# Optimization experiments

Hardware: AMD Instinct MI355X
Metric: run time of the kernel (lower is better)

## Reference

```python
import math
import jax, jax.numpy as jnp
import numpy as np

N_HEAD = 16
N_EMBD = 2048
HEAD_DIM = N_EMBD // N_HEAD  # 128
ROPE_BASE = 10000.0
EPS = 1e-12  # F.normalize eps


def setup_inputs() -> dict:
    key = jax.random.key(0)
    ks = jax.random.split(key, 5)
    B, T, C = 2, 2048, N_EMBD
    s = 0.02
    return {
        "x": jax.random.normal(ks[0], (B, T, C), jnp.float32),
        "Wq": jax.random.normal(ks[1], (C, C), jnp.float32) * s,
        "Wk": jax.random.normal(ks[2], (C, C), jnp.float32) * s,
        "Wv": jax.random.normal(ks[3], (C, C), jnp.float32) * s,
        "Wo": jax.random.normal(ks[4], (C, C), jnp.float32) * s,
        "qk_scale": jnp.ones((HEAD_DIM,), jnp.float32) / math.sqrt(N_EMBD),
    }


def _rope(x, cos, sin):
    # x: [B,T,H,D], cos/sin: [T, D/2] broadcast as [1,T,1,D/2]
    d = x.shape[-1] // 2
    x1, x2 = x[..., :d], x[..., d:]
    c = cos[None, :, None, :]
    s = sin[None, :, None, :]
    return jnp.concatenate([x1 * c + x2 * s, -x1 * s + x2 * c], axis=-1)


def reference(x, Wq, Wk, Wv, Wo, qk_scale):
    B, T, C = x.shape
    H, D = N_HEAD, HEAD_DIM

    q = (x @ Wq.T).reshape(B, T, H, D)
    k = (x @ Wk.T).reshape(B, T, H, D)
    v = (x @ Wv.T).reshape(B, T, H, D)

    # L2-normalize over head_dim, then per-channel scale (scaler() = param * sqrt(n_embd))
    scale_vec = qk_scale * math.sqrt(N_EMBD)  # == 1.0 at init
    q = scale_vec * (q / jnp.maximum(jnp.linalg.norm(q, axis=-1, keepdims=True), EPS))
    k = scale_vec * (k / jnp.maximum(jnp.linalg.norm(k, axis=-1, keepdims=True), EPS))

    # rotary embeddings (half-split, non-interleaved)
    inv_freq = 1.0 / (ROPE_BASE ** (jnp.arange(0, D, 2, dtype=jnp.float32) / D))
    freqs = jnp.arange(T, dtype=jnp.float32)[:, None] * inv_freq[None, :]  # [T, D/2]
    cos, sin = jnp.cos(freqs), jnp.sin(freqs)
    q = _rope(q, cos, sin)
    k = _rope(k, cos, sin)

    # causal SDPA with scale = sqrt(head_dim) (as in the source)
    scores = jnp.einsum("bthd,bshd->bhts", q, k) * math.sqrt(D)  # [B,H,T,T]
    causal = jnp.tril(jnp.ones((T, T), bool))
    scores = jnp.where(causal[None, None], scores, -jnp.inf)
    attn = jax.nn.softmax(scores, axis=-1)
    y = jnp.einsum("bhts,bshd->bthd", attn, v).reshape(B, T, C)
    return y @ Wo.T
```

## Files before the change

kernel.cpp:

```cpp
#include <hip/hip_runtime.h>
#include <math.h>

typedef _Float16 f16;
typedef _Float16 f16x2 __attribute__((ext_vector_type(2)));
typedef _Float16 f16x4 __attribute__((ext_vector_type(4)));
typedef _Float16 f16x8 __attribute__((ext_vector_type(8)));
typedef __fp16 fp16x2 __attribute__((ext_vector_type(2)));
typedef float f32x4 __attribute__((ext_vector_type(4)));
typedef float f32x16 __attribute__((ext_vector_type(16)));
typedef unsigned int u32;

#define T_ 2048
#define H_ 16
#define C_ 2048

__device__ __forceinline__ void gload_lds16(const f16* g, f16* l) {
  __builtin_amdgcn_global_load_lds((const __attribute__((address_space(1))) u32*)g,
                                   (__attribute__((address_space(3))) u32*)l, 16, 0, 0);
}

__device__ __forceinline__ u32 pkk(float x, float y) {
  union { fp16x2 h; u32 u; } z;
  z.h = __builtin_amdgcn_cvt_pkrtz(x, y);
  return z.u;
}

__global__ __launch_bounds__(256) void cast_all_kernel(
    const float* __restrict__ x, const float* __restrict__ wq, const float* __restrict__ wk,
    const float* __restrict__ wv, const float* __restrict__ wo,
    f16* __restrict__ xh, f16* __restrict__ wqh, f16* __restrict__ wkh,
    f16* __restrict__ wvh, f16* __restrict__ woh) {
  int b = blockIdx.x;
  const float* src; f16* dst; size_t off;
  if (b < 8192) { src = x; dst = xh; off = (size_t)b * 1024; }
  else {
    int s = (b - 8192) >> 12, bb = (b - 8192) & 4095;
    off = (size_t)bb * 1024;
    if (s == 0) { src = wq; dst = wqh; }
    else if (s == 1) { src = wk; dst = wkh; }
    else if (s == 2) { src = wv; dst = wvh; }
    else { src = wo; dst = woh; }
  }
  size_t i = off + (size_t)threadIdx.x * 4;
  float4 v = *(const float4*)&src[i];
  f16x4 o; o[0] = (f16)v.x; o[1] = (f16)v.y; o[2] = (f16)v.z; o[3] = (f16)v.w;
  *(f16x4*)&dst[i] = o;
}

template<typename OutT>
__device__ __forceinline__ void gemm128(const f16* __restrict__ A, const f16* __restrict__ Bm,
                                        OutT* __restrict__ Cm, f16* As, f16* Bs,
                                        int brow, int bcol) {
  const int K = 2048, N = 2048;
  const int tid = threadIdx.x, l = tid & 63, w = tid >> 6;
  const int lr = l & 15, lg = l >> 4;
  const int wr = (w >> 1) * 64, wc = (w & 1) * 64;
  const int srow = l >> 2, scol = (l & 3) * 8;
  const f16* gA0 = A + (size_t)(brow + w * 32 + srow) * K + scol;
  const f16* gA1 = gA0 + (size_t)16 * K;
  const f16* gB0 = Bm + (size_t)(bcol + w * 32 + srow) * K + scol;
  const f16* gB1 = gB0 + (size_t)16 * K;
  f16* lA0 = &As[(w * 32 + 0) * 32];
  f16* lA1 = &As[(w * 32 + 16) * 32];
  f16* lB0 = &Bs[(w * 32 + 0) * 32];
  f16* lB1 = &Bs[(w * 32 + 16) * 32];
  f32x4 acc[4][4] = {};
  for (int kt = 0; kt < K; kt += 32) {
    gload_lds16(gA0 + kt, lA0);
    gload_lds16(gA1 + kt, lA1);
    gload_lds16(gB0 + kt, lB0);
    gload_lds16(gB1 + kt, lB1);
    __syncthreads();
    f16x8 af[4], bf[4];
#pragma unroll
    for (int m = 0; m < 4; ++m) af[m] = *(const f16x8*)&As[(wr + m * 16 + lr) * 32 + lg * 8];
#pragma unroll
    for (int n = 0; n < 4; ++n) bf[n] = *(const f16x8*)&Bs[(wc + n * 16 + lr) * 32 + lg * 8];
#pragma unroll
    for (int m = 0; m < 4; ++m)
#pragma unroll
      for (int n = 0; n < 4; ++n)
        acc[m][n] = __builtin_amdgcn_mfma_f32_16x16x32_f16(af[m], bf[n], acc[m][n], 0, 0, 0);
    __syncthreads();
  }
#pragma unroll
  for (int m = 0; m < 4; ++m) {
    int row0 = brow + wr + m * 16 + lg * 4;
#pragma unroll
    for (int n = 0; n < 4; ++n) {
      int col = bcol + wc + n * 16 + lr;
#pragma unroll
      for (int j = 0; j < 4; ++j)
        Cm[(size_t)(row0 + j) * N + col] = (OutT)acc[m][n][j];
    }
  }
}

__global__ __launch_bounds__(256) void gemm_qkv_kernel(
    const f16* __restrict__ A, const f16* __restrict__ Wq, const f16* __restrict__ Wk,
    const f16* __restrict__ Wv, f16* __restrict__ Qo, f16* __restrict__ Ko, f16* __restrict__ Vo) {
  __shared__ f16 As[4096], Bs[4096];
  const f16* Bm; f16* Cm;
  if (blockIdx.z == 0) { Bm = Wq; Cm = Qo; }
  else if (blockIdx.z == 1) { Bm = Wk; Cm = Ko; }
  else { Bm = Wv; Cm = Vo; }
  gemm128<f16>(A, Bm, Cm, As, Bs, blockIdx.x * 128, blockIdx.y * 128);
}

__global__ __launch_bounds__(256) void gemm_out_kernel(
    const f16* __restrict__ A, const f16* __restrict__ Wo, float* __restrict__ Cm) {
  __shared__ f16 As[4096], Bs[4096];
  gemm128<float>(A, Wo, Cm, As, Bs, blockIdx.x * 128, blockIdx.y * 128);
}

__global__ __launch_bounds__(256) void normrope_kernel(f16* __restrict__ qp, f16* __restrict__ kp,
                                                       const float* __restrict__ qk_scale) {
  int w = threadIdx.x >> 6, l = threadIdx.x & 63;
  f16* q = blockIdx.y == 0 ? qp : kp;
  float fac = blockIdx.y == 0 ? 512.0f : 45.254833995939045f;
  int row = blockIdx.x * 4 + w;
  int t = (row >> 4) & (T_ - 1);
  size_t base = (size_t)row * 128;
  float x1 = (float)q[base + l], x2 = (float)q[base + 64 + l];
  float ss = x1 * x1 + x2 * x2;
#pragma unroll
  for (int m = 1; m < 64; m <<= 1) ss += __shfl_xor(ss, m);
  float inv = 1.0f / fmaxf(sqrtf(ss), 1e-12f);
  float sc1 = qk_scale[l] * fac;
  float sc2 = qk_scale[l + 64] * fac;
  float s1 = x1 * inv * sc1, s2 = x2 * inv * sc2;
  float invf = exp2f(-(float)l * 0.20762050593046013f);
  float ang = (float)t * invf;
  float sn, cs; sincosf(ang, &sn, &cs);
  q[base + l] = (f16)(s1 * cs + s2 * sn);
  q[base + 64 + l] = (f16)(-s1 * sn + s2 * cs);
}

#define KSTR 132
#define VSTR 68
__global__ __launch_bounds__(256, 2) void attn_kernel(
    const f16* __restrict__ Q, const f16* __restrict__ K, const f16* __restrict__ V,
    f16* __restrict__ Y) {
  __shared__ f16 Ks[2][64 * KSTR];
  __shared__ f16 Vt[2][128 * VSTR];
  const int tid = threadIdx.x, l = tid & 63, w = tid >> 6;
  const int lq = l & 31, hi = l >> 5;
  const int id = blockIdx.x;
  const int bh = id & 31;
  const int qi = id >> 5;
  const int qx = qi < 8 ? qi : 23 - qi;
  const int qb = qx * 128;
  const int b = bh >> 4, h = bh & 15;
  const size_t hb = ((size_t)b * T_ * H_ + h) * 128;
  const int qw = qb + w * 32;
  const int q = qw + lq;

  f16x8 qB[8];
  {
    const f16* qp = Q + hb + (size_t)q * 2048 + hi * 8;
#pragma unroll
    for (int dc = 0; dc < 8; ++dc) qB[dc] = *(const f16x8*)(qp + dc * 16);
  }

  const int ntiles = qb / 64 + 2;
  const int lastit = qb / 64 + (w >> 1);

  const int krow = tid >> 2, kcg = (tid & 3) * 32;
  const int vp2 = tid & 31, vdg = (tid >> 5) * 8;

  f16x8 kr0, kr1, kr2, kr3, vr0a, vr1a, vr0b, vr1b;
  auto load_tile = [&](int kv0) {
    const f16* ksrc = K + hb + (size_t)(kv0 + krow) * 2048 + kcg;
    kr0 = *(const f16x8*)(ksrc);
    kr1 = *(const f16x8*)(ksrc + 8);
    kr2 = *(const f16x8*)(ksrc + 16);
    kr3 = *(const f16x8*)(ksrc + 24);
    const f16* vsrc = V + hb + (size_t)(kv0 + 2 * vp2) * 2048;
    vr0a = *(const f16x8*)(vsrc + vdg);
    vr1a = *(const f16x8*)(vsrc + 2048 + vdg);
    vr0b = *(const f16x8*)(vsrc + vdg + 64);
    vr1b = *(const f16x8*)(vsrc + 2048 + vdg + 64);
  };
  auto write_tile = [&](int buf) {
    f16* kd = &Ks[buf][krow * KSTR + kcg];
    *(f16x8*)(kd) = kr0; *(f16x8*)(kd + 8) = kr1;
    *(f16x8*)(kd + 16) = kr2; *(f16x8*)(kd + 24) = kr3;
#pragma unroll
    for (int j = 0; j < 8; ++j) {
      union { f16x2 h2; u32 u; } p0, p1;
      p0.h2[0] = vr0a[j]; p0.h2[1] = vr1a[j];
      *(u32*)&Vt[buf][(vdg + j) * VSTR + 2 * vp2] = p0.u;
      p1.h2[0] = vr0b[j]; p1.h2[1] = vr1b[j];
      *(u32*)&Vt[buf][(vdg + 64 + j) * VSTR + 2 * vp2] = p1.u;
    }
  };

  load_tile(0);
  write_tile(0);
  __syncthreads();

  float mreg = -INFINITY, rsum = 0.f;
  f32x16 o0 = {}, o1 = {}, o2 = {}, o3 = {};

  for (int it = 0; it < ntiles; ++it) {
    const int cur = it & 1;
    const int kv0 = it * 64;
    const bool havenext = (it + 1 < ntiles);
    if (havenext) load_tile(kv0 + 64);

    if (it <= lastit) {
      f32x16 s0 = {}, s1 = {};
      const f16* kb = &Ks[cur][lq * KSTR + hi * 8];
#pragma unroll
      for (int dc = 0; dc < 8; ++dc) {
        f16x8 kf = *(const f16x8*)(kb + dc * 16);
        s0 = __builtin_amdgcn_mfma_f32_32x32x16_f16(kf, qB[dc], s0, 0, 0, 0);
      }
      const f16* kb1 = kb + 32 * KSTR;
#pragma unroll
      for (int dc = 0; dc < 8; ++dc) {
        f16x8 kf = *(const f16x8*)(kb1 + dc * 16);
        s1 = __builtin_amdgcn_mfma_f32_32x32x16_f16(kf, qB[dc], s1, 0, 0, 0);
      }
      if (it == lastit) {
#pragma unroll
        for (int r = 0; r < 16; ++r) {
          int crow = (r & 3) + 8 * (r >> 2) + 4 * hi;
          s0[r] = (kv0 + crow <= q) ? s0[r] : -INFINITY;
          s1[r] = (kv0 + 32 + crow <= q) ? s1[r] : -INFINITY;
        }
      }
      float pm = s0[0];
#pragma unroll
      for (int r = 1; r < 16; ++r) pm = fmaxf(pm, s0[r]);
#pragma unroll
      for (int r = 0; r < 16; ++r) pm = fmaxf(pm, s1[r]);
      pm = fmaxf(pm, __shfl_xor(pm, 32));
      if (__any(pm > mreg + 8.0f)) {
        float mn = fmaxf(mreg, pm);
        float al = __expf(mreg - mn);
        o0 *= al; o1 *= al; o2 *= al; o3 *= al;
        rsum *= al; mreg = mn;
      }
      float sum = 0.f;
#pragma unroll
      for (int r = 0; r < 16; ++r) { float e = __expf(s0[r] - mreg); s0[r] = e; sum += e; }
#pragma unroll
      for (int r = 0; r < 16; ++r) { float e = __expf(s1[r] - mreg); s1[r] = e; sum += e; }
      sum += __shfl_xor(sum, 32);
      rsum += sum;
#define PVSTEP(SV, BB, KS)                                                          \
      {                                                                             \
        u32 a0 = pkk(SV[8*BB+0], SV[8*BB+1]);                                       \
        u32 a1 = pkk(SV[8*BB+2], SV[8*BB+3]);                                       \
        u32 b0 = pkk(SV[8*BB+4], SV[8*BB+5]);                                       \
        u32 b1 = pkk(SV[8*BB+6], SV[8*BB+7]);                                       \
        u32 r0 = __shfl_xor(hi ? a0 : b0, 32);                                      \
        u32 r1 = __shfl_xor(hi ? a1 : b1, 32);                                      \
        union { u32 u[4]; f16x8 v; } pf;                                            \
        pf.u[0] = hi ? r0 : a0; pf.u[1] = hi ? r1 : a1;                             \
        pf.u[2] = hi ? b0 : r0; pf.u[3] = hi ? b1 : r1;                             \
        const f16* vb = &Vt[cur][lq * VSTR + (KS) * 16 + hi * 8];                   \
        o0 = __builtin_amdgcn_mfma_f32_32x32x16_f16(*(const f16x8*)(vb), pf.v, o0, 0, 0, 0); \
        o1 = __builtin_amdgcn_mfma_f32_32x32x16_f16(*(const f16x8*)(vb + 32 * VSTR), pf.v, o1, 0, 0, 0); \
        o2 = __builtin_amdgcn_mfma_f32_32x32x16_f16(*(const f16x8*)(vb + 64 * VSTR), pf.v, o2, 0, 0, 0); \
        o3 = __builtin_amdgcn_mfma_f32_32x32x16_f16(*(const f16x8*)(vb + 96 * VSTR), pf.v, o3, 0, 0, 0); \
      }
      PVSTEP(s0, 0, 0)
      PVSTEP(s0, 1, 1)
      PVSTEP(s1, 0, 2)
      PVSTEP(s1, 1, 3)
#undef PVSTEP
    }
    __syncthreads();
    if (havenext) {
      write_tile(cur ^ 1);
      __syncthreads();
    }
  }

  float inv = 1.0f / rsum;
  const size_t yb = ((size_t)(b * T_ + q)) * 2048 + h * 128;
#define OSTORE(OV, DT)                                                   \
  {                                                                      \
    _Pragma("unroll")                                                    \
    for (int g = 0; g < 4; ++g) {                                        \
      f16x4 pk;                                                          \
      pk[0] = (f16)(OV[g * 4 + 0] * inv); pk[1] = (f16)(OV[g * 4 + 1] * inv); \
      pk[2] = (f16)(OV[g * 4 + 2] * inv); pk[3] = (f16)(OV[g * 4 + 3] * inv); \
      *(f16x4*)&Y[yb + (DT) * 32 + g * 8 + 4 * hi] = pk;                 \
    }                                                                    \
  }
  OSTORE(o0, 0) OSTORE(o1, 1) OSTORE(o2, 2) OSTORE(o3, 3)
#undef OSTORE
}

extern "C" void kernel_launch(void* const* d_in, const int* in_sizes, int n_in,
                              void* d_out, int out_size, void* d_ws, size_t ws_size,
                              hipStream_t stream) {
  const float* x  = (const float*)d_in[0];
  const float* Wq = (const float*)d_in[1];
  const float* Wk = (const float*)d_in[2];
  const float* Wv = (const float*)d_in[3];
  const float* Wo = (const float*)d_in[4];
  const float* qk_scale = (const float*)d_in[5];
  float* out = (float*)d_out;
  char* ws = (char*)d_ws;

  f16* xh  = (f16*)(ws);
  f16* wqh = (f16*)(ws + 16777216);
  f16* wkh = (f16*)(ws + 25165824);
  f16* wvh = (f16*)(ws + 33554432);
  f16* woh = (f16*)(ws + 41943040);
  f16* qh  = (f16*)(ws + 50331648);
  f16* kh  = (f16*)(ws + 67108864);
  f16* vh  = (f16*)(ws + 83886080);
  f16* yh  = (f16*)(ws + 100663296);

  cast_all_kernel<<<dim3(24576), dim3(256), 0, stream>>>(x, Wq, Wk, Wv, Wo, xh, wqh, wkh, wvh, woh);
  gemm_qkv_kernel<<<dim3(32, 16, 3), dim3(256), 0, stream>>>(xh, wqh, wkh, wvh, qh, kh, vh);
  normrope_kernel<<<dim3(16384, 2), dim3(256), 0, stream>>>(qh, kh, qk_scale);
  attn_kernel<<<dim3(512), dim3(256), 0, stream>>>(qh, kh, vh, yh);
  gemm_out_kernel<<<dim3(32, 16), dim3(256), 0, stream>>>(yh, woh, out);
}
```

Measured before the change: 365.7 us.

## Split causal attention KV range into chunks and merge partial softmax results

Query tiles deep in the causal sequence now have their KV range split into 512-key chunks. Each chunk runs as its own block, which brings the attention grid from 512 to 1280 blocks of similar size. Chunks write unnormalized fp16 partial outputs plus per-row max and sum into reused workspace, and a new merge kernel combines them with log-sum-exp weights. To allow 4 blocks per CU, the LDS tiles drop from double to single buffering, and s_setprio hints now wrap the MFMA sections. The change adds an extra kernel launch, extra global traffic for the partial outputs, and fp16 rounding of those partials.

```diff
diff --git a/kernel.cpp b/kernel.cpp
--- a/kernel.cpp
+++ b/kernel.cpp
@@ -138,18 +138,33 @@
 
 #define KSTR 132
 #define VSTR 68
-__global__ __launch_bounds__(256, 2) void attn_kernel(
+__global__ __launch_bounds__(256, 4) void attn_kernel(
     const f16* __restrict__ Q, const f16* __restrict__ K, const f16* __restrict__ V,
-    f16* __restrict__ Y) {
-  __shared__ f16 Ks[2][64 * KSTR];
-  __shared__ f16 Vt[2][128 * VSTR];
+    f16* __restrict__ Y, f16* __restrict__ Op, float* __restrict__ ml) {
+  __shared__ f16 Ks[64 * KSTR];
+  __shared__ f16 Vt[128 * VSTR];
   const int tid = threadIdx.x, l = tid & 63, w = tid >> 6;
   const int lq = l & 31, hi = l >> 5;
-  const int id = blockIdx.x;
-  const int bh = id & 31;
-  const int qi = id >> 5;
-  const int qx = qi < 8 ? qi : 23 - qi;
-  const int qb = qx * 128;
+  const int bh = blockIdx.x / 40;
+  const int cidx = blockIdx.x - bh * 40;
+  int qi, j;
+  if (cidx < 4)       { qi = cidx;                  j = 0; }
+  else if (cidx < 12) { qi = 4 + ((cidx - 4) >> 1); j = (cidx - 4) & 1; }
+  else if (cidx < 24) { qi = 8 + (cidx - 12) / 3;   j = (cidx - 12) % 3; }
+  else                { qi = 12 + ((cidx - 24) >> 2); j = (cidx - 24) & 3; }
+  const int nch = (qi >> 2) + 1;
+  const bool multi = nch > 1;
+  const int qb = qi * 128;
+  const int s0kv = j * 512;
+  const int endkv = min(s0kv + 512, qb + 128);
+  const int nt = (endkv - s0kv) >> 6;
+  const int tbase = s0kv >> 6;
+  const int lastit = qi * 2 + (w >> 1);
+  int cid = 0;
+  if (multi) {
+    int pre = (qi < 8) ? (qi - 4) * 2 : (qi < 12 ? 8 + (qi - 8) * 3 : 20 + (qi - 12) * 4);
+    cid = bh * 36 + pre + j;
+  }
   const int b = bh >> 4, h = bh & 15;
   const size_t hb = ((size_t)b * T_ * H_ + h) * 128;
   const int qw = qb + w * 32;
@@ -161,9 +176,6 @@
 #pragma unroll
     for (int dc = 0; dc < 8; ++dc) qB[dc] = *(const f16x8*)(qp + dc * 16);
   }
-
-  const int ntiles = qb / 64 + 2;
-  const int lastit = qb / 64 + (w >> 1);
 
   const int krow = tid >> 2, kcg = (tid & 3) * 32;
   const int vp2 = tid & 31, vdg = (tid >> 5) * 8;
@@ -181,36 +193,37 @@
     vr0b = *(const f16x8*)(vsrc + vdg + 64);
     vr1b = *(const f16x8*)(vsrc + 2048 + vdg + 64);
   };
-  auto write_tile = [&](int buf) {
-    f16* kd = &Ks[buf][krow * KSTR + kcg];
+  auto write_tile = [&]() {
+    f16* kd = &Ks[krow * KSTR + kcg];
     *(f16x8*)(kd) = kr0; *(f16x8*)(kd + 8) = kr1;
     *(f16x8*)(kd + 16) = kr2; *(f16x8*)(kd + 24) = kr3;
 #pragma unroll
-    for (int j = 0; j < 8; ++j) {
+    for (int jj = 0; jj < 8; ++jj) {
       union { f16x2 h2; u32 u; } p0, p1;
-      p0.h2[0] = vr0a[j]; p0.h2[1] = vr1a[j];
-      *(u32*)&Vt[buf][(vdg + j) * VSTR + 2 * vp2] = p0.u;
-      p1.h2[0] = vr0b[j]; p1.h2[1] = vr1b[j];
-      *(u32*)&Vt[buf][(vdg + 64 + j) * VSTR + 2 * vp2] = p1.u;
+      p0.h2[0] = vr0a[jj]; p0.h2[1] = vr1a[jj];
+      *(u32*)&Vt[(vdg + jj) * VSTR + 2 * vp2] = p0.u;
+      p1.h2[0] = vr0b[jj]; p1.h2[1] = vr1b[jj];
+      *(u32*)&Vt[(vdg + 64 + jj) * VSTR + 2 * vp2] = p1.u;
     }
   };
 
-  load_tile(0);
-  write_tile(0);
+  load_tile(s0kv);
+  write_tile();
   __syncthreads();
 
   float mreg = -INFINITY, rsum = 0.f;
   f32x16 o0 = {}, o1 = {}, o2 = {}, o3 = {};
 
-  for (int it = 0; it < ntiles; ++it) {
-    const int cur = it & 1;
-    const int kv0 = it * 64;
-    const bool havenext = (it + 1 < ntiles);
+  for (int it = 0; it < nt; ++it) {
+    const int kv0 = s0kv + it * 64;
+    const bool havenext = (it + 1 < nt);
     if (havenext) load_tile(kv0 + 64);
 
-    if (it <= lastit) {
+    const int ti = tbase + it;
+    if (ti <= lastit) {
       f32x16 s0 = {}, s1 = {};
-      const f16* kb = &Ks[cur][lq * KSTR + hi * 8];
+      const f16* kb = &Ks[lq * KSTR + hi * 8];
+      __builtin_amdgcn_s_setprio(1);
 #pragma unroll
       for (int dc = 0; dc < 8; ++dc) {
         f16x8 kf = *(const f16x8*)(kb + dc * 16);
@@ -222,7 +235,8 @@
         f16x8 kf = *(const f16x8*)(kb1 + dc * 16);
         s1 = __builtin_amdgcn_mfma_f32_32x32x16_f16(kf, qB[dc], s1, 0, 0, 0);
       }
-      if (it == lastit) {
+      __builtin_amdgcn_s_setprio(0);
+      if (ti == lastit) {
 #pragma unroll
         for (int r = 0; r < 16; ++r) {
           int crow = (r & 3) + 8 * (r >> 2) + 4 * hi;
@@ -230,17 +244,24 @@
           s1[r] = (kv0 + 32 + crow <= q) ? s1[r] : -INFINITY;
         }
       }
-      float pm = s0[0];
-#pragma unroll
-      for (int r = 1; r < 16; ++r) pm = fmaxf(pm, s0[r]);
-#pragma unroll
-      for (int r = 0; r < 16; ++r) pm = fmaxf(pm, s1[r]);
-      pm = fmaxf(pm, __shfl_xor(pm, 32));
-      if (__any(pm > mreg + 8.0f)) {
+      float t8[8];
+#pragma unroll
+      for (int r = 0; r < 8; ++r) t8[r] = fmaxf(fmaxf(s0[r], s0[r + 8]), fmaxf(s1[r], s1[r + 8]));
+#pragma unroll
+      for (int off = 4; off > 0; off >>= 1)
+#pragma unroll
+        for (int r = 0; r < off; ++r) t8[r] = fmaxf(t8[r], t8[r + off]);
+      float pm = fmaxf(t8[0], __shfl_xor(t8[0], 32));
+      if (multi) {
         float mn = fmaxf(mreg, pm);
         float al = __expf(mreg - mn);
         o0 *= al; o1 *= al; o2 *= al; o3 *= al;
         rsum *= al; mreg = mn;
+      } else if (__any(pm > mreg + 8.0f)) {
+        float mn = fmaxf(mreg, pm);
+        float al = __expf(mreg - mn);
+        o0 *= al; o1 *= al; o2 *= al; o3 *= al;
+        rsum *= al; mreg = mn;
       }
       float sum = 0.f;
 #pragma unroll
@@ -249,6 +270,7 @@
       for (int r = 0; r < 16; ++r) { float e = __expf(s1[r] - mreg); s1[r] = e; sum += e; }
       sum += __shfl_xor(sum, 32);
       rsum += sum;
+      __builtin_amdgcn_s_setprio(1);
 #define PVSTEP(SV, BB, KS)                                                          \
       {                                                                             \
         u32 a0 = pkk(SV[8*BB+0], SV[8*BB+1]);                                       \
@@ -260,7 +282,7 @@
         union { u32 u[4]; f16x8 v; } pf;                                            \
         pf.u[0] = hi ? r0 : a0; pf.u[1] = hi ? r1 : a1;                             \
         pf.u[2] = hi ? b0 : r0; pf.u[3] = hi ? b1 : r1;                             \
-        const f16* vb = &Vt[cur][lq * VSTR + (KS) * 16 + hi * 8];                   \
+        const f16* vb = &Vt[lq * VSTR + (KS) * 16 + hi * 8];                        \
         o0 = __builtin_amdgcn_mfma_f32_32x32x16_f16(*(const f16x8*)(vb), pf.v, o0, 0, 0, 0); \
         o1 = __builtin_amdgcn_mfma_f32_32x32x16_f16(*(const f16x8*)(vb + 32 * VSTR), pf.v, o1, 0, 0, 0); \
         o2 = __builtin_amdgcn_mfma_f32_32x32x16_f16(*(const f16x8*)(vb + 64 * VSTR), pf.v, o2, 0, 0, 0); \
@@ -271,28 +293,97 @@
       PVSTEP(s1, 0, 2)
       PVSTEP(s1, 1, 3)
 #undef PVSTEP
+      __builtin_amdgcn_s_setprio(0);
     }
     __syncthreads();
     if (havenext) {
-      write_tile(cur ^ 1);
+      write_tile();
       __syncthreads();
     }
   }
 
-  float inv = 1.0f / rsum;
-  const size_t yb = ((size_t)(b * T_ + q)) * 2048 + h * 128;
+  if (!multi) {
+    float inv = 1.0f / rsum;
+    const size_t yb = ((size_t)(b * T_ + q)) * 2048 + h * 128;
 #define OSTORE(OV, DT)                                                   \
-  {                                                                      \
-    _Pragma("unroll")                                                    \
-    for (int g = 0; g < 4; ++g) {                                        \
-      f16x4 pk;                                                          \
-      pk[0] = (f16)(OV[g * 4 + 0] * inv); pk[1] = (f16)(OV[g * 4 + 1] * inv); \
-      pk[2] = (f16)(OV[g * 4 + 2] * inv); pk[3] = (f16)(OV[g * 4 + 3] * inv); \
-      *(f16x4*)&Y[yb + (DT) * 32 + g * 8 + 4 * hi] = pk;                 \
-    }                                                                    \
-  }
-  OSTORE(o0, 0) OSTORE(o1, 1) OSTORE(o2, 2) OSTORE(o3, 3)
+    {                                                                    \
+      _Pragma("unroll")                                                  \
+      for (int g = 0; g < 4; ++g) {                                      \
+        f16x4 pk;                                                        \
+        pk[0] = (f16)(OV[g * 4 + 0] * inv); pk[1] = (f16)(OV[g * 4 + 1] * inv); \
+        pk[2] = (f16)(OV[g * 4 + 2] * inv); pk[3] = (f16)(OV[g * 4 + 3] * inv); \
+        *(f16x4*)&Y[yb + (DT) * 32 + g * 8 + 4 * hi] = pk;               \
+      }                                                                  \
+    }
+    OSTORE(o0, 0) OSTORE(o1, 1) OSTORE(o2, 2) OSTORE(o3, 3)
 #undef OSTORE
+  } else {
+    const size_t ob = (size_t)cid * 16384 + (size_t)(w * 32 + lq) * 128;
+#define OSTORE(OV, DT)                                                   \
+    {                                                                    \
+      _Pragma("unroll")                                                  \
+      for (int g = 0; g < 4; ++g) {                                      \
+        f16x4 pk;                                                        \
+        pk[0] = (f16)OV[g * 4 + 0]; pk[1] = (f16)OV[g * 4 + 1];          \
+        pk[2] = (f16)OV[g * 4 + 2]; pk[3] = (f16)OV[g * 4 + 3];          \
+        *(f16x4*)&Op[ob + (DT) * 32 + g * 8 + 4 * hi] = pk;              \
+      }                                                                  \
+    }
+    OSTORE(o0, 0) OSTORE(o1, 1) OSTORE(o2, 2) OSTORE(o3, 3)
+#undef OSTORE
+    if (hi == 0) {
+      ml[(size_t)cid * 256 + (w * 32 + lq) * 2] = mreg;
+      ml[(size_t)cid * 256 + (w * 32 + lq) * 2 + 1] = rsum;
+    }
+  }
+}
+
+__global__ __launch_bounds__(256) void merge_kernel(const f16* __restrict__ Op,
+                                                    const float* __restrict__ ml,
+                                                    f16* __restrict__ Y) {
+  const int g = blockIdx.x;
+  const int bh = g / 12, qi = 4 + (g - 12 * (g / 12));
+  const int b = bh >> 4, h = bh & 15;
+  const int nch = (qi >> 2) + 1;
+  const int pre = (qi < 8) ? (qi - 4) * 2 : (qi < 12 ? 8 + (qi - 8) * 3 : 20 + (qi - 12) * 4);
+  const int cid0 = bh * 36 + pre;
+  const int row = threadIdx.x >> 1;
+  const int dh = (threadIdx.x & 1) * 64;
+  float mc[4], lc[4], wgt[4];
+  float M = -INFINITY;
+#pragma unroll
+  for (int c = 0; c < 4; ++c)
+    if (c < nch) {
+      mc[c] = ml[(size_t)(cid0 + c) * 256 + row * 2];
+      lc[c] = ml[(size_t)(cid0 + c) * 256 + row * 2 + 1];
+      M = fmaxf(M, mc[c]);
+    }
+  float lsum = 0.f;
+#pragma unroll
+  for (int c = 0; c < 4; ++c)
+    if (c < nch) { wgt[c] = __expf(mc[c] - M); lsum += lc[c] * wgt[c]; }
+  float inv = 1.0f / lsum;
+#pragma unroll
+  for (int c = 0; c < 4; ++c)
+    if (c < nch) wgt[c] *= inv;
+  const int t = qi * 128 + row;
+  const size_t yb = ((size_t)(b * T_ + t)) * 2048 + h * 128 + dh;
+  const size_t rb = (size_t)row * 128 + dh;
+#pragma unroll
+  for (int dblk = 0; dblk < 64; dblk += 8) {
+    float acc[8] = {};
+#pragma unroll
+    for (int c = 0; c < 4; ++c)
+      if (c < nch) {
+        f16x8 v = *(const f16x8*)&Op[(size_t)(cid0 + c) * 16384 + rb + dblk];
+#pragma unroll
+        for (int k = 0; k < 8; ++k) acc[k] += wgt[c] * (float)v[k];
+      }
+    f16x8 o;
+#pragma unroll
+    for (int k = 0; k < 8; ++k) o[k] = (f16)acc[k];
+    *(f16x8*)&Y[yb + dblk] = o;
+  }
 }
 
 extern "C" void kernel_launch(void* const* d_in, const int* in_sizes, int n_in,
@@ -316,10 +407,13 @@
   f16* kh  = (f16*)(ws + 67108864);
   f16* vh  = (f16*)(ws + 83886080);
   f16* yh  = (f16*)(ws + 100663296);
+  f16*   Op  = (f16*)(ws);
+  float* mlp = (float*)(ws + 37748736);
 
   cast_all_kernel<<<dim3(24576), dim3(256), 0, stream>>>(x, Wq, Wk, Wv, Wo, xh, wqh, wkh, wvh, woh);
   gemm_qkv_kernel<<<dim3(32, 16, 3), dim3(256), 0, stream>>>(xh, wqh, wkh, wvh, qh, kh, vh);
   normrope_kernel<<<dim3(16384, 2), dim3(256), 0, stream>>>(qh, kh, qk_scale);
-  attn_kernel<<<dim3(512), dim3(256), 0, stream>>>(qh, kh, vh, yh);
+  attn_kernel<<<dim3(1280), dim3(256), 0, stream>>>(qh, kh, vh, yh, Op, mlp);
+  merge_kernel<<<dim3(384), dim3(256), 0, stream>>>(Op, mlp, yh);
   gemm_out_kernel<<<dim3(32, 16), dim3(256), 0, stream>>>(yh, woh, out);
 }
```

Measured after the change: 694.4 us. +89.9%, slower.
